# Performance work log

Hardware: AMD Instinct MI355X
Metric: run time of the kernel (lower is better)

The kernel has to match this reference:

```python
import jax, jax.numpy as jnp
import numpy as np

HEAD_DIM = 128
N_HEADS = 32
N_KV_HEADS = 8
ROPE_BASE = 500000.0
QK_EPS = 1e-6


def _rope_cos_sin(position_ids, head_dim, base, dtype):
    # position_ids: [B, S] int -> cos/sin [B, 1, S, head_dim]
    inv_freq = 1.0 / (base ** (jnp.arange(0, head_dim, 2, dtype=jnp.float32) / head_dim))
    freqs = position_ids.astype(jnp.float32)[..., None] * inv_freq  # [B, S, D/2]
    emb = jnp.concatenate([freqs, freqs], axis=-1)  # [B, S, D]
    return jnp.cos(emb).astype(dtype)[:, None], jnp.sin(emb).astype(dtype)[:, None]


def _rotate_half(x):
    x1, x2 = jnp.split(x, 2, axis=-1)
    return jnp.concatenate([-x2, x1], axis=-1)


def _qk_norm(x, scale, eps):
    # L2 norm (not RMS): scale * x / (||x||_2 + eps)
    norm = jnp.sqrt(jnp.sum(x * x, axis=-1, keepdims=True))
    return scale * x / (norm + eps)


def setup_inputs() -> dict:
    key = jax.random.key(0)
    ks = jax.random.split(key, 7)
    B, S, H = 1, 2048, 4096
    kv_dim = N_KV_HEADS * HEAD_DIM
    return {
        "hidden_states": jax.random.normal(ks[0], (B, S, H), dtype=jnp.float32),
        "position_ids": jnp.broadcast_to(jnp.arange(S, dtype=jnp.int64 if jax.config.jax_enable_x64 else jnp.int32), (B, S)),
        "Wq": jax.random.normal(ks[1], (H, H), dtype=jnp.float32) * (H ** -0.5),
        "Wk": jax.random.normal(ks[2], (kv_dim, H), dtype=jnp.float32) * (H ** -0.5),
        "Wv": jax.random.normal(ks[3], (kv_dim, H), dtype=jnp.float32) * (H ** -0.5),
        "Wo": jax.random.normal(ks[4], (H, H), dtype=jnp.float32) * (H ** -0.5),
        "q_scale": jnp.ones((HEAD_DIM,), dtype=jnp.float32),
        "k_scale": jnp.ones((HEAD_DIM,), dtype=jnp.float32),
    }


def reference(hidden_states, position_ids, Wq, Wk, Wv, Wo, q_scale, k_scale):
    B, S, H = hidden_states.shape
    scaling = 1.0 / np.sqrt(HEAD_DIM)

    # projections (torch Linear: y = x @ W.T)
    q = (hidden_states @ Wq.T).reshape(B, S, N_HEADS, HEAD_DIM).transpose(0, 2, 1, 3)
    k = (hidden_states @ Wk.T).reshape(B, S, N_KV_HEADS, HEAD_DIM).transpose(0, 2, 1, 3)
    v = (hidden_states @ Wv.T).reshape(B, S, N_KV_HEADS, HEAD_DIM).transpose(0, 2, 1, 3)

    cos, sin = _rope_cos_sin(position_ids, HEAD_DIM, ROPE_BASE, q.dtype)
    q = q * cos + _rotate_half(q) * sin
    k = k * cos + _rotate_half(k) * sin

    q = _qk_norm(q, q_scale, QK_EPS)
    k = _qk_norm(k, k_scale, QK_EPS)

    # GQA: repeat kv heads to match query heads
    n_rep = N_HEADS // N_KV_HEADS
    k = jnp.repeat(k, n_rep, axis=1)  # [B, n_heads, S, D]
    v = jnp.repeat(v, n_rep, axis=1)

    # causal SDPA
    scores = jnp.einsum("bhqd,bhkd->bhqk", q, k) * scaling
    causal = jnp.tril(jnp.ones((S, S), dtype=bool))
    scores = jnp.where(causal, scores, jnp.finfo(scores.dtype).min)
    attn = jax.nn.softmax(scores, axis=-1)
    out = jnp.einsum("bhqk,bhkd->bhqd", attn, v)  # [B, H, S, D]

    out = out.transpose(0, 2, 1, 3).reshape(B, S, H)
    return out @ Wo.T
```

## Files before the change

kernel.cpp:

```cpp
#include <hip/hip_runtime.h>
#include <math.h>

typedef unsigned short u16;
typedef unsigned int u32;
typedef __attribute__((ext_vector_type(8))) short bf16x8;
typedef __attribute__((ext_vector_type(4))) float f32x4;

#define S_LEN 2048
#define HID 4096
#define NH 32
#define NKV 8
#define HD 128
#define QS 6144

__device__ __forceinline__ u16 f2bf(float f) {
  u32 u = __float_as_uint(f);
  u32 r = (u + 0x7FFFu + ((u >> 16) & 1u)) >> 16;
  return (u16)r;
}
__device__ __forceinline__ float bf2f(u16 v) {
  return __uint_as_float(((u32)v) << 16);
}
__device__ __forceinline__ f32x4 mfma16(bf16x8 a, bf16x8 b, f32x4 c) {
  return __builtin_amdgcn_mfma_f32_16x16x32_bf16(a, b, c, 0, 0, 0);
}
__device__ __forceinline__ void async16(const u16* g, u16* l) {
  __builtin_amdgcn_global_load_lds(
      (__attribute__((address_space(1))) void*)g,
      (__attribute__((address_space(3))) void*)l, 16, 0, 0);
}
#if __has_builtin(__builtin_amdgcn_exp2f)
#define EXP2(x) __builtin_amdgcn_exp2f(x)
#else
#define EXP2(x) exp2f(x)
#endif

#define VMC(n) asm volatile("s_waitcnt vmcnt(" #n ")" ::: "memory")
#define LGKM(n) asm volatile("s_waitcnt lgkmcnt(" #n ")" ::: "memory")
#define SB __builtin_amdgcn_sched_barrier(0)
#define BAR __builtin_amdgcn_s_barrier()
#define P1 __builtin_amdgcn_s_setprio(1)
#define P0 __builtin_amdgcn_s_setprio(0)

__global__ __launch_bounds__(256) void conv_all(
    const float* __restrict__ hs, const float* __restrict__ wq,
    const float* __restrict__ wk, const float* __restrict__ wv,
    const float* __restrict__ wo, u16* __restrict__ dhs, u16* __restrict__ dwq,
    u16* __restrict__ dwk, u16* __restrict__ dwv, u16* __restrict__ dwo) {
  int i = blockIdx.x * 256 + threadIdx.x;
  const float* src;
  u16* dst;
  int off;
  if (i < 2097152) { src = hs; dst = dhs; off = 0; }
  else if (i < 6291456) { src = wq; dst = dwq; off = 2097152; }
  else if (i < 7340032) { src = wk; dst = dwk; off = 6291456; }
  else if (i < 8388608) { src = wv; dst = dwv; off = 7340032; }
  else { src = wo; dst = dwo; off = 8388608; }
  int j = i - off;
  float4 v = ((const float4*)src)[j];
  ushort4 o;
  o.x = f2bf(v.x); o.y = f2bf(v.y); o.z = f2bf(v.z); o.w = f2bf(v.w);
  ((ushort4*)dst)[j] = o;
}


#define DSA(dst, qi, d)                                                    \
  {                                                                        \
    const u16* p_ = As + (d)*16384 + (wm * 64 + (qi)*32 + cl) * 64;        \
    _Pragma("unroll") for (int ii = 0; ii < 2; ii++)                       \
        _Pragma("unroll") for (int kk = 0; kk < 2; kk++)                   \
            dst[ii][kk] =                                                  \
        *(const bf16x8*)(p_ + ii * 1024 + ((c0 ^ (kk << 2)) << 3));        \
  }

#define DSB(dst, qj, d)                                                    \
  {                                                                        \
    const u16* p_ =                                                        \
        Bs + (d)*BSTR + (wn * (BN / 2) + (qj) * (BN / 4) + cl) * 64;       \
    _Pragma("unroll") for (int jj = 0; jj < NJ; jj++)                      \
        _Pragma("unroll") for (int kk = 0; kk < 2; kk++)                   \
            dst[jj][kk] =                                                  \
        *(const bf16x8*)(p_ + jj * 1024 + ((c0 ^ (kk << 2)) << 3));        \
  }

#define MM(qi, qj, asrc, bsrc)                                             \
  {                                                                        \
    _Pragma("unroll") for (int ii = 0; ii < 2; ii++)                       \
        _Pragma("unroll") for (int jj = 0; jj < NJ; jj++)                  \
            _Pragma("unroll") for (int kk = 0; kk < 2; kk++)               \
                acc[(qi)*2 + ii][(qj)*NJ + jj] =                           \
        mfma16(asrc[ii][kk], bsrc[jj][kk], acc[(qi)*2 + ii][(qj)*NJ + jj]);\
  }

#define LGKM_NB()                           \
  do {                                      \
    if constexpr (NJ == 3) LGKM(6);         \
    else LGKM(4);                           \
  } while (0)
#define LGKM_NB4()                          \
  do {                                      \
    if constexpr (NJ == 3) LGKM(10);        \
    else LGKM(8);                           \
  } while (0)
#define VMCNJ()                             \
  do {                                      \
    if constexpr (NJ == 3) VMC(3);          \
    else VMC(2);                            \
  } while (0)

template <int NJ>
__global__ __launch_bounds__(512, 2) void gemm8p(
    const u16* __restrict__ A, const u16* __restrict__ B,
    u16* __restrict__ Cb, float* __restrict__ Cf, int N, int K) {
  constexpr int BN = NJ * 64;
  constexpr int BSTR = BN * 64;
  extern __shared__ u16 lds[];
  u16* As = lds;
  u16* Bs = lds + 32768;
  const int tid = threadIdx.x;
  const int lane = tid & 63, wv = tid >> 6;
  const int cl = lane & 15, qd = lane >> 4;
  const int wm = wv >> 1, wn = wv & 1;
  const int c0 = qd ^ (cl & 7);

  const int cpx = gridDim.x >> 3;
  const int swz = (blockIdx.x & 7) * cpx + (blockIdx.x >> 3);
  const int m0 = (swz & 7) * 256;
  const int n0 = (swz >> 3) * BN;

  u32 aof[4], bof[NJ];
#pragma unroll
  for (int q = 0; q < 4; q++) {
    int r = q * 64 + wv * 8 + (lane >> 3);
    int c = (lane & 7) ^ (r & 7);
    aof[q] = (u32)(m0 + r) * K + c * 8;
  }
#pragma unroll
  for (int q = 0; q < NJ; q++) {
    int r = q * 64 + wv * 8 + (lane >> 3);
    int c = (lane & 7) ^ (r & 7);
    bof[q] = (u32)(n0 + r) * K + c * 8;
  }
  const int sbo = wv * 512;

  auto STA = [&](int tt, int d, int ra) {
    async16(A + (size_t)tt * 64 + aof[ra], As + d * 16384 + ra * 4096 + sbo);
  };
  auto STB = [&](int tt, int d, int rb) {
    async16(B + (size_t)tt * 64 + bof[rb], Bs + d * BSTR + rb * 4096 + sbo);
  };

  f32x4 acc[4][2 * NJ];
  f32x4 zz = {0.f, 0.f, 0.f, 0.f};
#pragma unroll
  for (int i = 0; i < 4; i++)
#pragma unroll
    for (int j = 0; j < 2 * NJ; j++) acc[i][j] = zz;
  bf16x8 A0r[2][2], A1r[2][2], B0r[NJ][2], B1r[NJ][2];

  const int NT = K >> 6;

  STA(0, 0, 0); STA(0, 0, 1); STA(0, 0, 2); STA(0, 0, 3);
  STB(0, 0, 0); STB(0, 0, 1);
  if constexpr (NJ == 3) STB(0, 0, 2);
  STB(1, 1, 0); STB(1, 1, 1);
  if constexpr (NJ == 3) STB(1, 1, 2);
  VMCNJ();
  SB;
  BAR;
  DSA(A0r, 0, 0); DSB(B0r, 0, 0);
  SB; LGKM(0); SB;

  for (int it = 0; it < (NT >> 1); ++it) {
    const int t = it * 2;
    const bool s2 = (t + 2) < NT;
    STA(t + 1, 1, 0); STA(t + 1, 1, 1);
    BAR; DSB(B1r, 1, 0); SB; LGKM_NB(); SB;
    P1; MM(0, 0, A0r, B0r); P0; SB; BAR;
    STA(t + 1, 1, 2); STA(t + 1, 1, 3);
    BAR; DSA(A1r, 1, 0); SB; LGKM(4); SB;
    P1; MM(0, 1, A0r, B1r); P0; SB; BAR;
    if (s2) { STB(t + 2, 0, 0); STB(t + 2, 0, 1); }
    BAR; SB; LGKM(0); SB;
    P1; MM(1, 0, A1r, B0r); P0; SB; BAR;
    if (s2) {
      if constexpr (NJ == 3) STB(t + 2, 0, 2);
      VMCNJ();
    } else {
      VMC(0);
    }
    BAR; DSB(B0r, 0, 1); DSA(A0r, 0, 1); SB; LGKM_NB4(); SB;
    P1; MM(1, 1, A1r, B1r); P0; SB; BAR;
    if (s2) { STA(t + 2, 0, 0); STA(t + 2, 0, 1); }
    BAR; DSB(B1r, 1, 1); SB; LGKM_NB(); SB;
    P1; MM(0, 0, A0r, B0r); P0; SB; BAR;
    if (s2) { STA(t + 2, 0, 2); STA(t + 2, 0, 3); }
    BAR; DSA(A1r, 1, 1); SB; LGKM(4); SB;
    P1; MM(0, 1, A0r, B1r); P0; SB; BAR;
    if (s2) { STB(t + 3, 1, 0); STB(t + 3, 1, 1); }
    BAR; SB; LGKM(0); SB;
    P1; MM(1, 0, A1r, B0r); P0; SB; BAR;
    if (s2) {
      if constexpr (NJ == 3) STB(t + 3, 1, 2);
      VMCNJ();
    } else {
      VMC(0);
    }
    BAR; DSB(B0r, 0, 0); DSA(A0r, 0, 0); SB; LGKM_NB4(); SB;
    P1; MM(1, 1, A1r, B1r); P0; SB; BAR;
  }

#pragma unroll
  for (int i = 0; i < 4; i++)
#pragma unroll
    for (int j = 0; j < 2 * NJ; j++) {
      int row = m0 + wm * 64 + i * 16 + qd * 4;
      int col = n0 + wn * (BN / 2) + (j / NJ) * (BN / 4) + (j % NJ) * 16 + cl;
#pragma unroll
      for (int r = 0; r < 4; r++) {
        float v = acc[i][j][r];
        if (Cb) Cb[(size_t)(row + r) * N + col] = f2bf(v);
        else    Cf[(size_t)(row + r) * N + col] = v;
      }
    }
}

__global__ __launch_bounds__(256) void rope_l2norm(
    u16* __restrict__ x, const int* __restrict__ pos_ids,
    const float* __restrict__ scale, int hmask, int hshift, int stride) {
  const int lane = threadIdx.x & 63;
  const int wv = threadIdx.x >> 6;
  const int idx = blockIdx.x * 4 + wv;
  const int s = idx >> hshift;
  const int h = idx & hmask;
  u16* p = x + (size_t)s * stride + h * HD;
  const float pos = (float)pos_ids[s];
  const float inv = expf((float)lane * -0.20503692777194264f);
  float sn, cs;
  sincosf(pos * inv, &sn, &cs);
  float a = bf2f(p[lane]);
  float b = bf2f(p[lane + 64]);
  float ra = a * cs - b * sn;
  float rb = b * cs + a * sn;
  float ss = ra * ra + rb * rb;
#pragma unroll
  for (int off = 32; off >= 1; off >>= 1) ss += __shfl_xor(ss, off, 64);
  float rd = 1.0f / (sqrtf(ss) + 1e-6f);
  p[lane] = f2bf(scale[lane] * ra * rd);
  p[lane + 64] = f2bf(scale[lane + 64] * rb * rd);
}

__global__ __launch_bounds__(256) void transpose_v(const u16* __restrict__ v,
                                                   u16* __restrict__ vt) {
  __shared__ u16 t[64][65];
  const int r = threadIdx.x >> 6;
  const int c = threadIdx.x & 63;
  const int s0 = blockIdx.x * 64, d0 = blockIdx.y * 64;
#pragma unroll
  for (int i = 0; i < 16; i++) {
    int row = i * 4 + r;
    t[row][c] = v[(size_t)(s0 + row) * QS + d0 + c];
  }
  __syncthreads();
#pragma unroll
  for (int i = 0; i < 16; i++) {
    int row = i * 4 + r;
    vt[(size_t)(d0 + row) * S_LEN + s0 + c] = t[c][row];
  }
}

#define PLD 68

__global__ __launch_bounds__(512) void flash_attn(
    const u16* __restrict__ QKV, const u16* __restrict__ Vt,
    u16* __restrict__ O) {
  extern __shared__ u16 alds[];
  u16* Ks = alds;
  u16* Vs = alds + 16384;
  u16* Ps = alds + 32768;
  const int tid = threadIdx.x;
  const int lane = tid & 63, wv = tid >> 6;
  const int cl = lane & 15, qd = lane >> 4;
  const int h = blockIdx.y;
  const int kvh = h >> 2;
  const float es = 0.12751629240081506f;

  const u16* Kbase = QKV + 4096 + kvh * HD;
  const u16* Vbase = Vt + (size_t)kvh * HD * S_LEN;

  auto stage = [&](int kt, int d) {
#pragma unroll
    for (int q = 0; q < 2; q++) {
      int c = q * 512 + wv * 64 + lane;
      int kr = c >> 4, kg = (c & 15) ^ (kr & 15);
      async16(Kbase + (size_t)(kt * 64 + kr) * QS + kg * 8,
              Ks + d * 8192 + (q * 512 + wv * 64) * 8);
      int vr = c >> 3, vg = (c & 7) ^ (vr & 7);
      async16(Vbase + (size_t)vr * S_LEN + kt * 64 + vg * 8,
              Vs + d * 8192 + (q * 512 + wv * 64) * 8);
    }
  };

  for (int half = 0; half < 2; half++) {
    const int qbi = half ? (15 - (int)blockIdx.x) : (int)blockIdx.x;
    const int q0 = qbi * 128;

    bf16x8 aQ[4];
    {
      const u16* qrow =
          QKV + (size_t)(q0 + wv * 16 + cl) * QS + h * HD + qd * 8;
#pragma unroll
      for (int kk = 0; kk < 4; kk++) aQ[kk] = *(const bf16x8*)(qrow + kk * 32);
    }

    f32x4 oacc[8];
    f32x4 zz = {0.f, 0.f, 0.f, 0.f};
#pragma unroll
    for (int n = 0; n < 8; n++) oacc[n] = zz;
    float lsum[4] = {0.f, 0.f, 0.f, 0.f};

    const int row_min = q0 + wv * 16;
    const int ktmax = 2 * qbi + 1;

    int cur = 0;
    stage(0, 0);
    for (int kt = 0; kt <= ktmax; kt++) {
      if (kt < ktmax) stage(kt + 1, cur ^ 1);
      if (kt == 0) {
        VMC(4);
        SB;
        BAR;
      }
      const int koff = cur * 8192;

      if (kt * 64 <= row_min + 15) {
        f32x4 sacc[4];
#pragma unroll
        for (int j = 0; j < 4; j++) sacc[j] = zz;
#pragma unroll
        for (int j = 0; j < 4; j++) {
          int row = j * 16 + cl;
#pragma unroll
          for (int kk = 0; kk < 4; kk++) {
            int ch = (kk * 4 + qd) ^ (row & 15);
            bf16x8 bK = *(const bf16x8*)&Ks[koff + row * 128 + ch * 8];
            sacc[j] = mfma16(aQ[kk], bK, sacc[j]);
          }
        }

        float pm[4][4];
        if (kt * 64 + 63 > row_min) {
          const int grow = row_min + qd * 4;
#pragma unroll
          for (int j = 0; j < 4; j++) {
            int gcol = kt * 64 + j * 16 + cl;
#pragma unroll
            for (int r = 0; r < 4; r++)
              pm[j][r] = (gcol <= grow + r) ? EXP2(sacc[j][r] * es) : 0.f;
          }
        } else {
#pragma unroll
          for (int j = 0; j < 4; j++)
#pragma unroll
            for (int r = 0; r < 4; r++) pm[j][r] = EXP2(sacc[j][r] * es);
        }
#pragma unroll
        for (int j = 0; j < 4; j++)
#pragma unroll
          for (int r = 0; r < 4; r++) lsum[r] += pm[j][r];

#pragma unroll
        for (int j = 0; j < 4; j++)
#pragma unroll
          for (int r = 0; r < 4; r++)
            Ps[(wv * 16 + qd * 4 + r) * PLD + j * 16 + cl] = f2bf(pm[j][r]);
        __asm__ volatile("s_waitcnt lgkmcnt(0)" ::: "memory");

#pragma unroll
        for (int kk = 0; kk < 2; kk++) {
          bf16x8 aP =
              *(const bf16x8*)&Ps[(wv * 16 + cl) * PLD + kk * 32 + qd * 8];
#pragma unroll
          for (int n = 0; n < 8; n++) {
            int row = n * 16 + cl;
            int ch = (kk * 4 + qd) ^ (row & 7);
            bf16x8 bV = *(const bf16x8*)&Vs[koff + row * 64 + ch * 8];
            oacc[n] = mfma16(aP, bV, oacc[n]);
          }
        }
      }

      VMC(0);
      SB;
      BAR;
      cur ^= 1;
    }

#pragma unroll
    for (int r = 0; r < 4; r++) {
#pragma unroll
      for (int off = 8; off >= 1; off >>= 1)
        lsum[r] += __shfl_xor(lsum[r], off, 64);
    }
#pragma unroll
    for (int r = 0; r < 4; r++) {
      float il = 1.0f / lsum[r];
      int row = row_min + qd * 4 + r;
#pragma unroll
      for (int n = 0; n < 8; n++)
        O[(size_t)row * HID + h * HD + n * 16 + cl] = f2bf(oacc[n][r] * il);
    }
  }
}

extern "C" void kernel_launch(void* const* d_in, const int* in_sizes, int n_in,
                              void* d_out, int out_size, void* d_ws, size_t ws_size,
                              hipStream_t stream) {
  const float* hs = (const float*)d_in[0];
  const int* pos = (const int*)d_in[1];
  const float* Wq = (const float*)d_in[2];
  const float* Wk = (const float*)d_in[3];
  const float* Wv = (const float*)d_in[4];
  const float* Wo = (const float*)d_in[5];
  const float* qsc = (const float*)d_in[6];
  const float* ksc = (const float*)d_in[7];
  float* out = (float*)d_out;
  char* ws = (char*)d_ws;
  const size_t MB = 1u << 20;

  u16* hs_b  = (u16*)(ws + 0 * MB);
  u16* wq_b  = (u16*)(ws + 16 * MB);
  u16* wk_b  = (u16*)(ws + 48 * MB);
  u16* wv_b  = (u16*)(ws + 56 * MB);
  u16* qkv_b = (u16*)(ws + 64 * MB);
  u16* vt_b  = (u16*)(ws + 88 * MB);
  u16* wo_b  = (u16*)(ws + 92 * MB);
  u16* o_b   = hs_b;

  static bool attr_set = false;
  if (!attr_set) {
    hipFuncSetAttribute(reinterpret_cast<const void*>(&gemm8p<3>),
                        hipFuncAttributeMaxDynamicSharedMemorySize, 114688);
    hipFuncSetAttribute(reinterpret_cast<const void*>(&gemm8p<2>),
                        hipFuncAttributeMaxDynamicSharedMemorySize, 98304);
    hipFuncSetAttribute(reinterpret_cast<const void*>(&flash_attn),
                        hipFuncAttributeMaxDynamicSharedMemorySize, 82944);
    attr_set = true;
  }

  conv_all<<<49152, 256, 0, stream>>>(hs, Wq, Wk, Wv, Wo,
                                      hs_b, wq_b, wk_b, wv_b, wo_b);

  gemm8p<3><<<dim3(8 * (QS / 192)), 512, 114688, stream>>>(
      hs_b, wq_b, qkv_b, nullptr, QS, HID);

  rope_l2norm<<<S_LEN * NH / 4, 256, 0, stream>>>(qkv_b, pos, qsc, NH - 1, 5, QS);
  rope_l2norm<<<S_LEN * NKV / 4, 256, 0, stream>>>(qkv_b + 4096, pos, ksc, NKV - 1, 3, QS);
  transpose_v<<<dim3(S_LEN / 64, (NKV * HD) / 64), 256, 0, stream>>>(qkv_b + 5120, vt_b);

  flash_attn<<<dim3(8, NH), 512, 82944, stream>>>(qkv_b, vt_b, o_b);

  gemm8p<2><<<dim3(8 * (HID / 128)), 512, 98304, stream>>>(
      o_b, wo_b, nullptr, out, HID, HID);
}
```

Measured before the change: 465.8 us.

## Restructure GEMM main loop from 8-phase to 4-phase schedule

Replaces the 8-phase interleaved load/compute schedule of the bf16 MFMA GEMM with a 4-phase one. Each phase now issues all A or B tile loads for a k-step at once and runs two MFMA sub-blocks per barrier pair, which halves the barrier count per iteration. The trade-off is coarser overlap: LDS reads are waited on fully (lgkmcnt 0) before each phase, and the outstanding global-load accounting changes to a fixed VMC(4). That wait count looks suspicious for the NJ=3 case and may expose memory latency or mis-synchronize.

Measured after the change: 457.3 us. About the same (-1.8%).

```diff
diff --git a/kernel.cpp b/kernel.cpp
--- a/kernel.cpp
+++ b/kernel.cpp
@@ -92,24 +92,14 @@
         mfma16(asrc[ii][kk], bsrc[jj][kk], acc[(qi)*2 + ii][(qj)*NJ + jj]);\
   }
 
-#define LGKM_NB()                           \
-  do {                                      \
-    if constexpr (NJ == 3) LGKM(6);         \
-    else LGKM(4);                           \
-  } while (0)
-#define LGKM_NB4()                          \
-  do {                                      \
-    if constexpr (NJ == 3) LGKM(10);        \
-    else LGKM(8);                           \
-  } while (0)
-#define VMCNJ()                             \
-  do {                                      \
-    if constexpr (NJ == 3) VMC(3);          \
-    else VMC(2);                            \
-  } while (0)
+#define PH2(MMA1, MMA2)                                          \
+  {                                                              \
+    BAR; LGKM(0); SB;                                            \
+    P1; MMA1; MMA2; P0; SB; BAR;                                 \
+  }
 
 template <int NJ>
-__global__ __launch_bounds__(512, 2) void gemm8p(
+__global__ __launch_bounds__(512, 2) void gemm4p(
     const u16* __restrict__ A, const u16* __restrict__ B,
     u16* __restrict__ Cb, float* __restrict__ Cf, int N, int K) {
   constexpr int BN = NJ * 64;
@@ -143,11 +133,15 @@
   }
   const int sbo = wv * 512;
 
-  auto STA = [&](int tt, int d, int ra) {
-    async16(A + (size_t)tt * 64 + aof[ra], As + d * 16384 + ra * 4096 + sbo);
+  auto STAll = [&](int tt, int d) {
+#pragma unroll
+    for (int q = 0; q < 4; q++)
+      async16(A + (size_t)tt * 64 + aof[q], As + d * 16384 + q * 4096 + sbo);
   };
-  auto STB = [&](int tt, int d, int rb) {
-    async16(B + (size_t)tt * 64 + bof[rb], Bs + d * BSTR + rb * 4096 + sbo);
+  auto STBall = [&](int tt, int d) {
+#pragma unroll
+    for (int q = 0; q < NJ; q++)
+      async16(B + (size_t)tt * 64 + bof[q], Bs + d * BSTR + q * 4096 + sbo);
   };
 
   f32x4 acc[4][2 * NJ];
@@ -160,54 +154,36 @@
 
   const int NT = K >> 6;
 
-  STA(0, 0, 0); STA(0, 0, 1); STA(0, 0, 2); STA(0, 0, 3);
-  STB(0, 0, 0); STB(0, 0, 1);
-  if constexpr (NJ == 3) STB(0, 0, 2);
-  STB(1, 1, 0); STB(1, 1, 1);
-  if constexpr (NJ == 3) STB(1, 1, 2);
-  VMCNJ();
+  STAll(0, 0); STBall(0, 0); STAll(1, 1);
+  VMC(4);
   SB;
   BAR;
-  DSA(A0r, 0, 0); DSB(B0r, 0, 0);
-  SB; LGKM(0); SB;
 
   for (int it = 0; it < (NT >> 1); ++it) {
     const int t = it * 2;
     const bool s2 = (t + 2) < NT;
-    STA(t + 1, 1, 0); STA(t + 1, 1, 1);
-    BAR; DSB(B1r, 1, 0); SB; LGKM_NB(); SB;
-    P1; MM(0, 0, A0r, B0r); P0; SB; BAR;
-    STA(t + 1, 1, 2); STA(t + 1, 1, 3);
-    BAR; DSA(A1r, 1, 0); SB; LGKM(4); SB;
-    P1; MM(0, 1, A0r, B1r); P0; SB; BAR;
-    if (s2) { STB(t + 2, 0, 0); STB(t + 2, 0, 1); }
-    BAR; SB; LGKM(0); SB;
-    P1; MM(1, 0, A1r, B0r); P0; SB; BAR;
+    DSA(A0r, 0, 0); DSA(A1r, 1, 0); DSB(B0r, 0, 0);
+    STBall(t + 1, 1);
+    PH2(MM(0, 0, A0r, B0r), MM(1, 0, A1r, B0r));
+    DSB(B1r, 1, 0);
     if (s2) {
-      if constexpr (NJ == 3) STB(t + 2, 0, 2);
-      VMCNJ();
+      STAll(t + 2, 0);
+      VMC(4);
     } else {
       VMC(0);
     }
-    BAR; DSB(B0r, 0, 1); DSA(A0r, 0, 1); SB; LGKM_NB4(); SB;
-    P1; MM(1, 1, A1r, B1r); P0; SB; BAR;
-    if (s2) { STA(t + 2, 0, 0); STA(t + 2, 0, 1); }
-    BAR; DSB(B1r, 1, 1); SB; LGKM_NB(); SB;
-    P1; MM(0, 0, A0r, B0r); P0; SB; BAR;
-    if (s2) { STA(t + 2, 0, 2); STA(t + 2, 0, 3); }
-    BAR; DSA(A1r, 1, 1); SB; LGKM(4); SB;
-    P1; MM(0, 1, A0r, B1r); P0; SB; BAR;
-    if (s2) { STB(t + 3, 1, 0); STB(t + 3, 1, 1); }
-    BAR; SB; LGKM(0); SB;
-    P1; MM(1, 0, A1r, B0r); P0; SB; BAR;
+    PH2(MM(0, 1, A0r, B1r), MM(1, 1, A1r, B1r));
+    DSA(A0r, 0, 1); DSA(A1r, 1, 1); DSB(B0r, 0, 1);
+    if (s2) STBall(t + 2, 0);
+    PH2(MM(0, 0, A0r, B0r), MM(1, 0, A1r, B0r));
+    DSB(B1r, 1, 1);
     if (s2) {
-      if constexpr (NJ == 3) STB(t + 3, 1, 2);
-      VMCNJ();
+      STAll(t + 3, 1);
+      VMC(4);
     } else {
       VMC(0);
     }
-    BAR; DSB(B0r, 0, 0); DSA(A0r, 0, 0); SB; LGKM_NB4(); SB;
-    P1; MM(1, 1, A1r, B1r); P0; SB; BAR;
+    PH2(MM(0, 1, A0r, B1r), MM(1, 1, A1r, B1r));
   }
 
 #pragma unroll
@@ -439,9 +415,9 @@
 
   static bool attr_set = false;
   if (!attr_set) {
-    hipFuncSetAttribute(reinterpret_cast<const void*>(&gemm8p<3>),
+    hipFuncSetAttribute(reinterpret_cast<const void*>(&gemm4p<3>),
                         hipFuncAttributeMaxDynamicSharedMemorySize, 114688);
-    hipFuncSetAttribute(reinterpret_cast<const void*>(&gemm8p<2>),
+    hipFuncSetAttribute(reinterpret_cast<const void*>(&gemm4p<2>),
                         hipFuncAttributeMaxDynamicSharedMemorySize, 98304);
     hipFuncSetAttribute(reinterpret_cast<const void*>(&flash_attn),
                         hipFuncAttributeMaxDynamicSharedMemorySize, 82944);
@@ -451,7 +427,7 @@
   conv_all<<<49152, 256, 0, stream>>>(hs, Wq, Wk, Wv, Wo,
                                       hs_b, wq_b, wk_b, wv_b, wo_b);
 
-  gemm8p<3><<<dim3(8 * (QS / 192)), 512, 114688, stream>>>(
+  gemm4p<3><<<dim3(8 * (QS / 192)), 512, 114688, stream>>>(
       hs_b, wq_b, qkv_b, nullptr, QS, HID);
 
   rope_l2norm<<<S_LEN * NH / 4, 256, 0, stream>>>(qkv_b, pos, qsc, NH - 1, 5, QS);
@@ -460,6 +436,6 @@
 
   flash_attn<<<dim3(8, NH), 512, 82944, stream>>>(qkv_b, vt_b, o_b);
 
-  gemm8p<2><<<dim3(8 * (HID / 128)), 512, 98304, stream>>>(
+  gemm4p<2><<<dim3(8 * (HID / 128)), 512, 98304, stream>>>(
       o_b, wo_b, nullptr, out, HID, HID);
 }
```
